# Optimization experiments

Measured on AMD Instinct MI355X. Metric: run time of the kernel, lower is better.

## Reference

```python
import jax, jax.numpy as jnp
import numpy as np

N, X_DIM, Y_DIM, HID = 1024, 128, 128, 256


def setup_inputs() -> dict:
    key = jax.random.key(0)
    k1, k2, k3, k4 = jax.random.split(key, 4)
    return {
        "x_samples": jax.random.normal(k1, (N, X_DIM), dtype=jnp.float32),
        "y_samples": jax.random.normal(k2, (N, Y_DIM), dtype=jnp.float32),
        "W1": jax.random.normal(k3, (X_DIM + Y_DIM, HID), dtype=jnp.float32) * 0.05,
        "b1": jnp.zeros((HID,), dtype=jnp.float32),
        "W2": jax.random.normal(k4, (HID, 1), dtype=jnp.float32) * 0.05,
        "b2": jnp.zeros((1,), dtype=jnp.float32),
    }


def reference(x_samples, y_samples, W1, b1, W2, b2):
    n = y_samples.shape[0]
    x_dim = x_samples.shape[-1]
    # Split first linear so we never materialize the N^2 concat:
    W1x, W1y = W1[:x_dim], W1[x_dim:]
    pre_x = x_samples @ W1x  # [N, H]
    pre_y = y_samples @ W1y  # [N, H]
    # T0: F on matched pairs (x_i, y_i)
    T0 = jax.nn.relu(pre_x + pre_y + b1) @ W2 + b2  # [N, 1]
    # T1[i, j] = F([x_j, y_i]) - 1.0  (all-pairs grid)
    h = jax.nn.relu(pre_x[None, :, :] + pre_y[:, None, :] + b1)  # [N, N, H]
    T1 = h @ W2 + b2 - 1.0  # [N, N, 1]
    lse = jax.nn.logsumexp(T1, axis=1)  # [N, 1]
    lower_bound = T0.mean() - jnp.exp(lse - jnp.log(jnp.float32(n))).mean()
    return lower_bound
```

## Files before the change

kernel.cpp:

```cpp
#include <hip/hip_runtime.h>

typedef _Float16 h2 __attribute__((ext_vector_type(2)));
typedef unsigned int u32;

#define OFF_W2H  0xA0000u
#define OFF_A2   0x100000u
#define OFF_C2   0x180000u

__device__ __forceinline__ u32 pack2(float a, float b) {
  h2 v; v.x = (_Float16)a; v.y = (_Float16)b;
  return __builtin_bit_cast(u32, v);
}
__device__ __forceinline__ h2 as_h2(u32 u) { return __builtin_bit_cast(h2, u); }

__device__ __forceinline__ h2 cvt2(float a, float b) {
#if __has_builtin(__builtin_amdgcn_cvt_pkrtz)
  return __builtin_bit_cast(h2, __builtin_amdgcn_cvt_pkrtz(a, b));
#else
  h2 v; v.x = (_Float16)a; v.y = (_Float16)b; return v;
#endif
}
__device__ __forceinline__ float fdot2(h2 a, h2 b, float c) {
#if __has_builtin(__builtin_amdgcn_fdot2)
  return __builtin_amdgcn_fdot2(a, b, c, false);
#else
  return (float)a.x * (float)b.x + (float)a.y * (float)b.y + c;
#endif
}
__device__ __forceinline__ h2 relu2(h2 t) {
  h2 z; z.x = (_Float16)0.0f; z.y = (_Float16)0.0f;
  return __builtin_elementwise_max(t, z);
}

__global__ __launch_bounds__(256) void k1_pre(const float* __restrict__ x,
                                              const float* __restrict__ y,
                                              const float* __restrict__ W1,
                                              const float* __restrict__ b1,
                                              const float* __restrict__ W2,
                                              u32* __restrict__ wsu,
                                              float* __restrict__ out) {
  const int b = blockIdx.x, tid = threadIdx.x;
  if (b == 256) {
    if (tid < 128) wsu[(OFF_W2H >> 2) + tid] = pack2(W2[2 * tid], W2[2 * tid + 1]);
    if (tid == 128) out[0] = 0.0f;
    return;
  }
  const int mat = b >> 7;
  const int idx = b & 127, ht = idx & 7, rt = idx >> 3;
  const int tx = tid & 15, ty = tid >> 4;
  const int h0 = ht * 32 + tx * 2;
  const int r0 = rt * 64 + ty * 4;
  const float* src = (mat ? y : x) + r0 * 128;
  const float* w1p = W1 + (mat ? 128 * 256 : 0) + h0;
  u32* dst = wsu + ((mat ? OFF_C2 : OFF_A2) >> 2) + ht * 16 + tx;

  float acc0[4], acc1[4];
  float bx = 0.0f, by = 0.0f;
  if (mat) { const float2 bv = *(const float2*)(b1 + h0); bx = bv.x; by = bv.y; }
#pragma unroll
  for (int i = 0; i < 4; ++i) { acc0[i] = bx; acc1[i] = by; }

#pragma unroll 4
  for (int kk = 0; kk < 64; ++kk) {
    const float2 wA = *(const float2*)(w1p + (2 * kk) * 256);
    const float2 wB = *(const float2*)(w1p + (2 * kk + 1) * 256);
    const h2 w0 = cvt2(wA.x, wB.x);
    const h2 w1h = cvt2(wA.y, wB.y);
#pragma unroll
    for (int i = 0; i < 4; ++i) {
      const float2 xv = *(const float2*)(src + i * 128 + 2 * kk);
      const h2 xh = cvt2(xv.x, xv.y);
      acc0[i] = fdot2(xh, w0, acc0[i]);
      acc1[i] = fdot2(xh, w1h, acc1[i]);
    }
  }
#pragma unroll
  for (int i = 0; i < 4; ++i) {
    const int R = r0 + i;
    dst[(R >> 5) * 4096 + (R & 31) * 128] = pack2(acc0[i], acc1[i]);
  }
}

__global__ __launch_bounds__(256, 1) void k2_main(const u32* __restrict__ wsu,
                                                  const float* __restrict__ B2,
                                                  float* __restrict__ out) {
  const int bi = blockIdx.x >> 4, bj = blockIdx.x & 15;
  const int tid = threadIdx.x;
  const int tx = tid & 15, ty = tid >> 4;

  __shared__ uint4 sA4[64 * 32];
  __shared__ uint4 sC4[64 * 32];
  __shared__ float sred[4];

  {
    const u32* gA = wsu + (OFF_A2 >> 2) + bj * 8192;
    const u32* gC = wsu + (OFF_C2 >> 2) + bi * 8192;
    const int j = tid >> 3, t8 = tid & 7;
#pragma unroll
    for (int half = 0; half < 2; ++half) {
      const int row = j + 32 * half;
      const int sw = (row >> 2) & 7;
#pragma unroll
      for (int m = 0; m < 4; ++m) {
        const int q = t8 + 8 * m;
        sA4[row * 32 + (q ^ sw)] = *(const uint4*)(gA + row * 128 + q * 4);
        sC4[row * 32 + (q ^ sw)] = *(const uint4*)(gC + row * 128 + q * 4);
      }
    }
  }
  __syncthreads();

  const uint4* pA = sA4 + (tx * 4) * 32;
  const uint4* pC = sC4 + (ty * 4) * 32;
  const uint4* pW = (const uint4*)(wsu + (OFF_W2H >> 2));
  const int swzA = tx & 7, swzC = ty & 7;

  float acc[16];
#pragma unroll
  for (int p = 0; p < 16; ++p) acc[p] = 0.0f;

#pragma unroll 2
  for (int g = 0; g < 32; ++g) {
    const uint4 av0 = pA[0 * 32 + (g ^ swzA)];
    const uint4 av1 = pA[1 * 32 + (g ^ swzA)];
    const uint4 av2 = pA[2 * 32 + (g ^ swzA)];
    const uint4 av3 = pA[3 * 32 + (g ^ swzA)];
    const uint4 cv0 = pC[0 * 32 + (g ^ swzC)];
    const uint4 cv1 = pC[1 * 32 + (g ^ swzC)];
    const uint4 cv2 = pC[2 * 32 + (g ^ swzC)];
    const uint4 cv3 = pC[3 * 32 + (g ^ swzC)];
    const uint4 wv = pW[g];
    const u32 ww[4] = {wv.x, wv.y, wv.z, wv.w};
    const u32 aa[4][4] = {{av0.x, av0.y, av0.z, av0.w},
                          {av1.x, av1.y, av1.z, av1.w},
                          {av2.x, av2.y, av2.z, av2.w},
                          {av3.x, av3.y, av3.z, av3.w}};
    const u32 cc[4][4] = {{cv0.x, cv0.y, cv0.z, cv0.w},
                          {cv1.x, cv1.y, cv1.z, cv1.w},
                          {cv2.x, cv2.y, cv2.z, cv2.w},
                          {cv3.x, cv3.y, cv3.z, cv3.w}};
#pragma unroll
    for (int m = 0; m < 4; ++m) {
      const h2 w = as_h2(ww[m]);
#pragma unroll
      for (int ii = 0; ii < 4; ++ii) {
        const h2 ci = as_h2(cc[ii][m]);
#pragma unroll
        for (int jj = 0; jj < 4; ++jj) {
          acc[ii * 4 + jj] = fdot2(relu2(as_h2(aa[jj][m]) + ci), w, acc[ii * 4 + jj]);
        }
      }
    }
  }

  const float b2 = B2[0];
  float val = 0.0f;
#pragma unroll
  for (int p = 0; p < 16; ++p) val += __expf(acc[p] + (b2 - 1.0f));
  val *= -1.0f / 1048576.0f;
  if (bi == bj && tx == ty) {
    float d = 0.0f;
#pragma unroll
    for (int c = 0; c < 4; ++c) d += acc[c * 5];
    val += (d + 4.0f * b2) * (1.0f / 1024.0f);
  }
#pragma unroll
  for (int off = 32; off > 0; off >>= 1) val += __shfl_down(val, off, 64);
  if ((tid & 63) == 0) sred[tid >> 6] = val;
  __syncthreads();
  if (tid == 0) atomicAdd(out, sred[0] + sred[1] + sred[2] + sred[3]);
}

extern "C" void kernel_launch(void* const* d_in, const int* in_sizes, int n_in,
                              void* d_out, int out_size, void* d_ws, size_t ws_size,
                              hipStream_t stream) {
  const float* x  = (const float*)d_in[0];
  const float* y  = (const float*)d_in[1];
  const float* W1 = (const float*)d_in[2];
  const float* b1 = (const float*)d_in[3];
  const float* W2 = (const float*)d_in[4];
  const float* b2 = (const float*)d_in[5];
  u32* wsu = (u32*)d_ws;

  hipLaunchKernelGGL(k1_pre, dim3(257), dim3(256), 0, stream, x, y, W1, b1, W2,
                     wsu, (float*)d_out);
  hipLaunchKernelGGL(k2_main, dim3(256), dim3(256), 0, stream, wsu, b2,
                     (float*)d_out);
}
```

Measured before the change: 95.46 us.

## Read C operand from global memory, store A transposed in LDS, raise occupancy

The C (pre_y) operand is no longer staged in shared memory. Each thread reads its C rows straight from global memory, where 16 threads of a row group share addresses and so hit cache. The A tile is stored in LDS in a transposed layout so that consecutive threads read consecutive uint4 entries with no XOR swizzle, and the k1 output layout is simplified to match. LDS use drops by half and the launch bound no longer forces one block per CU, which should allow more waves per CU. In exchange the inner loop now waits on global/L2 latency for C, which may stall despite the deeper unroll.

```diff
diff --git a/kernel.cpp b/kernel.cpp
--- a/kernel.cpp
+++ b/kernel.cpp
@@ -77,58 +77,50 @@
 #pragma unroll
   for (int i = 0; i < 4; ++i) {
     const int R = r0 + i;
-    dst[(R >> 5) * 4096 + (R & 31) * 128] = pack2(acc0[i], acc1[i]);
+    dst[R * 128] = pack2(acc0[i], acc1[i]);
   }
 }
 
-__global__ __launch_bounds__(256, 1) void k2_main(const u32* __restrict__ wsu,
-                                                  const float* __restrict__ B2,
-                                                  float* __restrict__ out) {
+__global__ __launch_bounds__(256) void k2_main(const u32* __restrict__ wsu,
+                                               const float* __restrict__ B2,
+                                               float* __restrict__ out) {
   const int bi = blockIdx.x >> 4, bj = blockIdx.x & 15;
   const int tid = threadIdx.x;
   const int tx = tid & 15, ty = tid >> 4;
 
-  __shared__ uint4 sA4[64 * 32];
-  __shared__ uint4 sC4[64 * 32];
+  __shared__ uint4 sA4[32 * 64];
   __shared__ float sred[4];
 
   {
     const u32* gA = wsu + (OFF_A2 >> 2) + bj * 8192;
-    const u32* gC = wsu + (OFF_C2 >> 2) + bi * 8192;
-    const int j = tid >> 3, t8 = tid & 7;
+    const int row = tid & 63, qb = (tid >> 6) * 8;
+    const int pr = (row >> 2) | ((row & 3) << 4);
 #pragma unroll
-    for (int half = 0; half < 2; ++half) {
-      const int row = j + 32 * half;
-      const int sw = (row >> 2) & 7;
-#pragma unroll
-      for (int m = 0; m < 4; ++m) {
-        const int q = t8 + 8 * m;
-        sA4[row * 32 + (q ^ sw)] = *(const uint4*)(gA + row * 128 + q * 4);
-        sC4[row * 32 + (q ^ sw)] = *(const uint4*)(gC + row * 128 + q * 4);
-      }
+    for (int m = 0; m < 8; ++m) {
+      const int q = qb + m;
+      sA4[q * 64 + pr] = *(const uint4*)(gA + row * 128 + q * 4);
     }
   }
   __syncthreads();
 
-  const uint4* pA = sA4 + (tx * 4) * 32;
-  const uint4* pC = sC4 + (ty * 4) * 32;
+  const uint4* pA = sA4 + tx;
+  const uint4* gC = (const uint4*)(wsu + (OFF_C2 >> 2)) + (bi * 64 + ty * 4) * 32;
   const uint4* pW = (const uint4*)(wsu + (OFF_W2H >> 2));
-  const int swzA = tx & 7, swzC = ty & 7;
 
   float acc[16];
 #pragma unroll
   for (int p = 0; p < 16; ++p) acc[p] = 0.0f;
 
-#pragma unroll 2
+#pragma unroll 4
   for (int g = 0; g < 32; ++g) {
-    const uint4 av0 = pA[0 * 32 + (g ^ swzA)];
-    const uint4 av1 = pA[1 * 32 + (g ^ swzA)];
-    const uint4 av2 = pA[2 * 32 + (g ^ swzA)];
-    const uint4 av3 = pA[3 * 32 + (g ^ swzA)];
-    const uint4 cv0 = pC[0 * 32 + (g ^ swzC)];
-    const uint4 cv1 = pC[1 * 32 + (g ^ swzC)];
-    const uint4 cv2 = pC[2 * 32 + (g ^ swzC)];
-    const uint4 cv3 = pC[3 * 32 + (g ^ swzC)];
+    const uint4 av0 = pA[g * 64 + 0];
+    const uint4 av1 = pA[g * 64 + 16];
+    const uint4 av2 = pA[g * 64 + 32];
+    const uint4 av3 = pA[g * 64 + 48];
+    const uint4 cv0 = gC[0 * 32 + g];
+    const uint4 cv1 = gC[1 * 32 + g];
+    const uint4 cv2 = gC[2 * 32 + g];
+    const uint4 cv3 = gC[3 * 32 + g];
     const uint4 wv = pW[g];
     const u32 ww[4] = {wv.x, wv.y, wv.z, wv.w};
     const u32 aa[4][4] = {{av0.x, av0.y, av0.z, av0.w},
```

After: 99.36 us. +4.1%, slower.
